# Performance work log

Measured on AMD Instinct MI355X. Metric: run time of the kernel, lower is better.

The kernel has to match this reference:

```python
import jax, jax.numpy as jnp
import numpy as np

C = 64
K = 3  # kernel_size
B, H, W = 8, 128, 128


def conv2d(x, w, b, pad, groups=1):
    y = jax.lax.conv_general_dilated(
        x, w, window_strides=(1, 1), padding=[(pad, pad), (pad, pad)],
        feature_group_count=groups, dimension_numbers=('NCHW', 'OIHW', 'NCHW'))
    return y + b[None, :, None, None]


def setup_inputs() -> dict:
    key = jax.random.key(0)
    ks = jax.random.split(key, 11)
    s3 = 1.0 / np.sqrt(C * 9)  # kaiming-ish scale for 3x3 convs
    inp = {
        'x':  jax.random.normal(ks[0], (B, C, H, W), jnp.float32),
        'w0': jax.random.normal(ks[1], (C, C, 3, 3), jnp.float32) * s3,
        'b0': jax.random.normal(ks[2], (C,), jnp.float32) * 0.01,
        'w1': jax.random.normal(ks[3], (C, 1, 3, 3), jnp.float32) * (1.0 / 3.0),  # depthwise
        'b1': jax.random.normal(ks[4], (C,), jnp.float32) * 0.01,
        'w2': jax.random.normal(ks[5], (1, 1, K), jnp.float32) * (1.0 / np.sqrt(K)),  # conv1d over channel axis
        'b2': jax.random.normal(ks[6], (1,), jnp.float32) * 0.01,
        'w3': jax.random.normal(ks[7], (C * K * K, C, 1, 1), jnp.float32) * (1.0 / np.sqrt(C)),  # 1x1 -> dynamic filters
        'b3': jax.random.normal(ks[8], (C * K * K,), jnp.float32) * 0.01,
        'wf': jax.random.normal(ks[9], (C, C, 3, 3), jnp.float32) * s3,
        'bf': jax.random.normal(ks[10], (C,), jnp.float32) * 0.01,
    }
    return inp


def reference(x, w0, b0, w1, b1, w2, b2, w3, b3, wf, bf):
    b, c, h, w = x.shape
    pre = x
    # conv0: dense 3x3
    x0 = conv2d(x, w0, b0, pad=1)
    # conv1: depthwise 3x3
    x1 = conv2d(x0, w1, b1, pad=1, groups=c)
    # ECA-style channel attention: global avg pool -> conv1d over channel dim
    m = jnp.mean(x0, axis=(2, 3))  # [b, c]
    x2 = jax.lax.conv_general_dilated(
        m[:, None, :], w2, window_strides=(1,), padding=[(K // 2, K // 2)],
        dimension_numbers=('NCH', 'OIH', 'NCH')) + b2[None, :, None]  # [b, 1, c]
    out = x1 + x2[:, 0, :, None, None]  # broadcast [b,c,1,1] over h,w
    # conv3: 1x1 producing per-pixel dynamic filters [b, c*9, h, w]
    fil = jnp.einsum('oc,bchw->bohw', w3[:, :, 0, 0], out) + b3[None, :, None, None]
    filter_x = fil.reshape(b, c, K * K, h, w)
    # unfold(x0): 3x3 patches, channel-major then row-major kernel positions
    xp = jnp.pad(x0, ((0, 0), (0, 0), (1, 1), (1, 1)))
    unfold_x = jnp.stack(
        [xp[:, :, i:i + h, j:j + w] for i in range(3) for j in range(3)], axis=2)  # [b,c,9,h,w]
    out = jnp.sum(unfold_x * filter_x, axis=2)  # per-pixel dynamic conv
    out = jnp.where(out >= 0, out, 0.2 * out)  # LeakyReLU(0.2)
    out = conv2d(out, wf, bf, pad=1) + pre
    return out
```

## Files before the change

kernel.cpp:

```cpp
#include <hip/hip_runtime.h>

#define BB 8
#define C 64
#define HH 128
#define WW 128
#define HW (HH*WW)

#define TS 72
#define NPX 324

typedef __attribute__((ext_vector_type(8))) short short8;
typedef __attribute__((ext_vector_type(4))) short short4v;
typedef __attribute__((ext_vector_type(4))) float f32x4;

__device__ inline unsigned short f2bf(float f) {
    union { float f; unsigned u; } v; v.f = f;
    unsigned r = v.u + 0x7fff + ((v.u >> 16) & 1);
    return (unsigned short)(r >> 16);
}
__device__ inline float bf2f(unsigned short h) {
    union { unsigned u; float f; } v; v.u = ((unsigned)h) << 16;
    return v.f;
}

__global__ __launch_bounds__(256) void prep_kernel(
    const float* __restrict__ w0, const float* __restrict__ wf,
    const float* __restrict__ w3, const float* __restrict__ b3,
    unsigned short* __restrict__ wb0, unsigned short* __restrict__ wbf,
    unsigned short* __restrict__ wb3, float* __restrict__ b3r,
    float* __restrict__ m)
{
    const int t = blockIdx.x * 256 + threadIdx.x;
    for (int i = t; i < C*C*9; i += 32*256) {
        int p = i % 9; int rest = i / 9; int ci = rest % C; int oc = rest / C;
        wb0[(p*C + oc)*C + ci] = f2bf(w0[i]);
        wbf[(p*C + oc)*C + ci] = f2bf(wf[i]);
    }
    for (int i = t; i < 9*C*C; i += 32*256) {
        int j = i >> 12, oc = (i >> 6) & 63, k = i & 63;
        wb3[i] = f2bf(w3[(oc*9 + j)*C + k]);
    }
    for (int i = t; i < 9*C; i += 32*256) {
        int j = i >> 6, oc = i & 63;
        b3r[i] = b3[oc*9 + j];
    }
    for (int i = t; i < BB*C; i += 32*256) m[i] = 0.f;
}

__global__ __launch_bounds__(512) void conv0_kernel(
    const float* __restrict__ x,
    const unsigned short* __restrict__ wb,
    const float* __restrict__ bias,
    unsigned short* __restrict__ x0g)
{
    __shared__ unsigned short tile[NPX*TS];
    const int b  = blockIdx.z;
    const int h0 = blockIdx.y * 16;
    const int w0 = blockIdx.x * 16;
    const int t  = threadIdx.x;

    {
        const int pxi = t & 63, g = t >> 6;
        for (int px = pxi; px < NPX; px += 64) {
            int th = px / 18, tw = px - th*18;
            int gh = h0 + th - 1, gw = w0 + tw - 1;
            short8 v = {0,0,0,0,0,0,0,0};
            if ((unsigned)gh < HH && (unsigned)gw < WW) {
                const float* sp = x + ((size_t)(b*C + g*8)*HW + gh*WW + gw);
#pragma unroll
                for (int k = 0; k < 8; ++k) v[k] = (short)f2bf(sp[k*HW]);
            }
            *(short8*)&tile[px*TS + g*8] = v;
        }
    }
    __syncthreads();

    const int wid = t >> 6, ln = t & 63;
    const int l15 = ln & 15, q = ln >> 4;

    f32x4 acc[2][4];
#pragma unroll
    for (int nt = 0; nt < 2; ++nt)
#pragma unroll
        for (int mt = 0; mt < 4; ++mt) acc[nt][mt] = (f32x4){0.f,0.f,0.f,0.f};

#pragma unroll
    for (int p = 0; p < 9; ++p) {
        const int dh = p / 3, dw = p % 3;
#pragma unroll
        for (int ks = 0; ks < 2; ++ks) {
            short8 af[4];
#pragma unroll
            for (int mt = 0; mt < 4; ++mt)
                af[mt] = *(const short8*)&wb[((size_t)(p*C) + mt*16 + l15)*C + ks*32 + q*8];
            short8 bf[2];
#pragma unroll
            for (int nt = 0; nt < 2; ++nt)
                bf[nt] = *(const short8*)&tile[((wid*2+nt+dh)*18 + l15 + dw)*TS + ks*32 + q*8];
#pragma unroll
            for (int nt = 0; nt < 2; ++nt)
#pragma unroll
                for (int mt = 0; mt < 4; ++mt)
                    acc[nt][mt] = __builtin_amdgcn_mfma_f32_16x16x32_bf16(
                        af[mt], bf[nt], acc[nt][mt], 0, 0, 0);
        }
    }

#pragma unroll
    for (int nt = 0; nt < 2; ++nt) {
        const int hh = h0 + wid*2 + nt;
        const size_t base = ((size_t)(b*HW) + hh*WW + w0 + l15)*C;
#pragma unroll
        for (int mt = 0; mt < 4; ++mt) {
            const int oc0 = mt*16 + q*4;
            const float4 bv = *(const float4*)&bias[oc0];
            unsigned u0 = (unsigned)f2bf(acc[nt][mt][0] + bv.x)
                        | ((unsigned)f2bf(acc[nt][mt][1] + bv.y) << 16);
            unsigned u1 = (unsigned)f2bf(acc[nt][mt][2] + bv.z)
                        | ((unsigned)f2bf(acc[nt][mt][3] + bv.w) << 16);
            uint2 uu; uu.x = u0; uu.y = u1;
            *(uint2*)&x0g[base + oc0] = uu;
        }
    }
}

__global__ __launch_bounds__(256) void mean_kernel(
    const unsigned short* __restrict__ x0, float* __restrict__ m)
{
    const int b = blockIdx.x >> 4, slice = blockIdx.x & 15;
    const int t = threadIdx.x;
    const int pxi = t >> 3, g = t & 7;
    const unsigned short* base = x0 + ((size_t)b*HW + slice*1024)*C + g*8;
    float s[8];
#pragma unroll
    for (int k = 0; k < 8; ++k) s[k] = 0.f;
    for (int it = 0; it < 32; ++it) {
        short8 v = *(const short8*)&base[(size_t)(it*32 + pxi)*C];
#pragma unroll
        for (int k = 0; k < 8; ++k) s[k] += bf2f((unsigned short)v[k]);
    }
    __shared__ float red[32][64];
#pragma unroll
    for (int k = 0; k < 8; ++k) red[pxi][g*8+k] = s[k];
    __syncthreads();
    if (t < 64) {
        float acc = 0.f;
        for (int i = 0; i < 32; ++i) acc += red[i][t];
        atomicAdd(&m[b*C + t], acc * (1.f/(float)HW));
    }
}

__global__ __launch_bounds__(512) void fused_dyn_kernel(
    const unsigned short* __restrict__ x0,
    const float* __restrict__ w1, const float* __restrict__ b1,
    const float* __restrict__ w2, const float* __restrict__ b2,
    const unsigned short* __restrict__ wb3,
    const float* __restrict__ b3r,
    const float* __restrict__ m,
    unsigned short* __restrict__ yg)
{
    __shared__ unsigned short tile[NPX*TS];
    __shared__ unsigned short alds[256*64];
    const int b  = blockIdx.z;
    const int h0 = blockIdx.y * 16;
    const int w0 = blockIdx.x * 16;
    const int t  = threadIdx.x;

    {
        const int pxi = t & 63, g = t >> 6;
        for (int px = pxi; px < NPX; px += 64) {
            int th = px / 18, tw = px - th*18;
            int gh = h0 + th - 1, gw = w0 + tw - 1;
            short8 v = {0,0,0,0,0,0,0,0};
            if ((unsigned)gh < HH && (unsigned)gw < WW)
                v = *(const short8*)&x0[((size_t)(b*HW) + gh*WW + gw)*C + g*8];
            *(short8*)&tile[px*TS + g*8] = v;
        }
    }
    __syncthreads();

    {
        const int px = t & 255, ghalf = t >> 8;
        const int r = px >> 4, cc = px & 15;
        const unsigned short* tb = tile + (r*18 + cc)*TS;
        const float w2a = w2[0], w2b = w2[1], w2c = w2[2], b2v = b2[0];
        const int sw = px & 7;
#pragma unroll
        for (int g = 0; g < 4; ++g) {
            const int octet = ghalf*4 + g;
            float dw8[8];
#pragma unroll
            for (int k = 0; k < 8; ++k) dw8[k] = 0.f;
#pragma unroll
            for (int j = 0; j < 9; ++j) {
                short8 v = *(const short8*)&tb[((j/3)*18 + (j%3))*TS + octet*8];
#pragma unroll
                for (int k = 0; k < 8; ++k)
                    dw8[k] = fmaf(w1[(octet*8+k)*9 + j],
                                  bf2f((unsigned short)v[k]), dw8[k]);
            }
            short8 o;
#pragma unroll
            for (int k = 0; k < 8; ++k) {
                const int c = octet*8 + k;
                const float mc = m[b*C + c];
                const float mp = (c > 0)  ? m[b*C + c - 1] : 0.f;
                const float mn = (c < 63) ? m[b*C + c + 1] : 0.f;
                const float att = fmaf(w2a, mp, fmaf(w2b, mc, fmaf(w2c, mn, b2v)));
                o[k] = (short)f2bf(dw8[k] + b1[c] + att);
            }
            *(short8*)&alds[px*64 + ((octet ^ sw) * 8)] = o;
        }
    }
    __syncthreads();

    const int wid = t >> 6, ln = t & 63;
    const int l15 = ln & 15, q = ln >> 4;
    const int rl0 = (wid & 3) * 4;
    const int ogh = wid >> 2;

    short8 pfrag[4][2];
#pragma unroll
    for (int nt = 0; nt < 4; ++nt) {
        const int p = (rl0 + nt)*16 + l15;
        const int psw = p & 7;
#pragma unroll
        for (int ks = 0; ks < 2; ++ks)
            pfrag[nt][ks] = *(const short8*)&alds[p*64 + (((ks*4 + q) ^ psw) * 8)];
    }

#pragma unroll
    for (int ogi = 0; ogi < 2; ++ogi) {
        const int og = ogh*2 + ogi;
        f32x4 yac[4];
#pragma unroll
        for (int nt = 0; nt < 4; ++nt) yac[nt] = (f32x4){0.f,0.f,0.f,0.f};

        for (int j = 0; j < 9; ++j) {
            const int dh = j / 3, dw = j - dh*3;
            const f32x4 seed = *(const f32x4*)&b3r[j*64 + og*16 + q*4];
            const size_t abase = ((size_t)(j*64 + og*16 + l15))*C;
            const short8 a0 = *(const short8*)&wb3[abase + q*8];
            const short8 a1 = *(const short8*)&wb3[abase + 32 + q*8];
#pragma unroll
            for (int nt = 0; nt < 4; ++nt) {
                f32x4 fil = __builtin_amdgcn_mfma_f32_16x16x32_bf16(
                    a0, pfrag[nt][0], seed, 0, 0, 0);
                fil = __builtin_amdgcn_mfma_f32_16x16x32_bf16(
                    a1, pfrag[nt][1], fil, 0, 0, 0);
                const short4v pv = *(const short4v*)
                    &tile[((rl0+nt+dh)*18 + l15 + dw)*TS + og*16 + q*4];
#pragma unroll
                for (int reg = 0; reg < 4; ++reg)
                    yac[nt][reg] = fmaf(fil[reg],
                        bf2f((unsigned short)pv[reg]), yac[nt][reg]);
            }
        }

#pragma unroll
        for (int nt = 0; nt < 4; ++nt) {
            const size_t base = ((size_t)(b*HW) + (h0+rl0+nt)*WW + w0 + l15)*C;
            f32x4 v = yac[nt];
#pragma unroll
            for (int reg = 0; reg < 4; ++reg)
                v[reg] = (v[reg] >= 0.f) ? v[reg] : 0.2f * v[reg];
            unsigned u0 = (unsigned)f2bf(v[0]) | ((unsigned)f2bf(v[1]) << 16);
            unsigned u1 = (unsigned)f2bf(v[2]) | ((unsigned)f2bf(v[3]) << 16);
            uint2 uu; uu.x = u0; uu.y = u1;
            *(uint2*)&yg[base + og*16 + q*4] = uu;
        }
    }
}

__global__ __launch_bounds__(512) void convf_kernel(
    const unsigned short* __restrict__ yg,
    const unsigned short* __restrict__ wb,
    const float* __restrict__ bias,
    const float* __restrict__ res,
    float* __restrict__ outg)
{
    __shared__ unsigned short tile[NPX*TS];
    const int b  = blockIdx.z;
    const int h0 = blockIdx.y * 16;
    const int w0 = blockIdx.x * 16;
    const int t  = threadIdx.x;

    {
        const int pxi = t & 63, g = t >> 6;
        for (int px = pxi; px < NPX; px += 64) {
            int th = px / 18, tw = px - th*18;
            int gh = h0 + th - 1, gw = w0 + tw - 1;
            short8 v = {0,0,0,0,0,0,0,0};
            if ((unsigned)gh < HH && (unsigned)gw < WW)
                v = *(const short8*)&yg[((size_t)(b*HW) + gh*WW + gw)*C + g*8];
            *(short8*)&tile[px*TS + g*8] = v;
        }
    }
    __syncthreads();

    const int wid = t >> 6, ln = t & 63;
    const int l15 = ln & 15, q = ln >> 4;

    f32x4 acc[2][4];
#pragma unroll
    for (int mg = 0; mg < 2; ++mg)
#pragma unroll
        for (int nt = 0; nt < 4; ++nt) acc[mg][nt] = (f32x4){0.f,0.f,0.f,0.f};

#pragma unroll
    for (int p = 0; p < 9; ++p) {
        const int dh = p / 3, dw = p % 3;
#pragma unroll
        for (int ks = 0; ks < 2; ++ks) {
            short8 bfrag[4];
#pragma unroll
            for (int nt = 0; nt < 4; ++nt)
                bfrag[nt] = *(const short8*)&wb[((size_t)(p*C) + nt*16 + l15)*C + ks*32 + q*8];
            short8 afrag[2];
#pragma unroll
            for (int mg = 0; mg < 2; ++mg)
                afrag[mg] = *(const short8*)&tile[((wid*2+mg+dh)*18 + l15 + dw)*TS + ks*32 + q*8];
#pragma unroll
            for (int mg = 0; mg < 2; ++mg)
#pragma unroll
                for (int nt = 0; nt < 4; ++nt)
                    acc[mg][nt] = __builtin_amdgcn_mfma_f32_16x16x32_bf16(
                        afrag[mg], bfrag[nt], acc[mg][nt], 0, 0, 0);
        }
    }

#pragma unroll
    for (int mg = 0; mg < 2; ++mg) {
        const int hh = h0 + wid*2 + mg;
#pragma unroll
        for (int nt = 0; nt < 4; ++nt) {
            const int oc = nt*16 + l15;
            const float bv = bias[oc];
            const size_t base = (size_t)(b*C + oc)*HW + hh*WW + w0 + q*4;
            const float4 rv = *(const float4*)&res[base];
            float4 ov;
            ov.x = acc[mg][nt][0] + bv + rv.x;
            ov.y = acc[mg][nt][1] + bv + rv.y;
            ov.z = acc[mg][nt][2] + bv + rv.z;
            ov.w = acc[mg][nt][3] + bv + rv.w;
            *(float4*)&outg[base] = ov;
        }
    }
}

extern "C" void kernel_launch(void* const* d_in, const int* in_sizes, int n_in,
                              void* d_out, int out_size, void* d_ws, size_t ws_size,
                              hipStream_t stream) {
    const float* x  = (const float*)d_in[0];
    const float* w0 = (const float*)d_in[1];
    const float* b0 = (const float*)d_in[2];
    const float* w1 = (const float*)d_in[3];
    const float* b1 = (const float*)d_in[4];
    const float* w2 = (const float*)d_in[5];
    const float* b2 = (const float*)d_in[6];
    const float* w3 = (const float*)d_in[7];
    const float* b3 = (const float*)d_in[8];
    const float* wf = (const float*)d_in[9];
    const float* bf = (const float*)d_in[10];
    float* out = (float*)d_out;

    unsigned short* x0  = (unsigned short*)d_ws;
    unsigned short* y   = x0  + (size_t)BB*HW*C;
    float*          m   = (float*)(y + (size_t)BB*HW*C);
    unsigned short* wb0 = (unsigned short*)(m + BB*C);
    unsigned short* wbf = wb0 + 9*C*C;
    unsigned short* wb3 = wbf + 9*C*C;
    float*          b3r = (float*)(wb3 + 9*C*C);

    prep_kernel<<<32, 256, 0, stream>>>(w0, wf, w3, b3, wb0, wbf, wb3, b3r, m);
    conv0_kernel<<<dim3(8,8,8), 512, 0, stream>>>(x, wb0, b0, x0);
    mean_kernel<<<128, 256, 0, stream>>>(x0, m);
    fused_dyn_kernel<<<dim3(8,8,8), 512, 0, stream>>>(
        x0, w1, b1, w2, b2, wb3, b3r, m, y);
    convf_kernel<<<dim3(8,8,8), 512, 0, stream>>>(y, wbf, bf, x, out);
}
```

Measured before the change: 246.5 us.

## Fuse channel mean into conv0, pre-convert input to NHWC bf16, retile convf

Adds a separate kernel that converts the NCHW fp32 input into NHWC bf16, so conv0 loads its halo tile with one vectorised read per pixel instead of eight strided fp32 reads. The channel-mean reduction moves into the conv0 epilogue using wave shuffles and an LDS reduction, which removes the standalone mean kernel and its re-read of x0. The sum is scaled by 1/HW later in the dynamic kernel. The final conv switches to 8x32 tiles so residual loads and output stores are contiguous across 32 columns, at the cost of a slightly larger halo tile and an extra pass over the input.

Result: no change. 248.2 us (+0.7%).

```diff
diff --git a/kernel.cpp b/kernel.cpp
--- a/kernel.cpp
+++ b/kernel.cpp
@@ -8,6 +8,7 @@
 
 #define TS 72
 #define NPX 324
+#define FNPX 340
 
 typedef __attribute__((ext_vector_type(8))) short short8;
 typedef __attribute__((ext_vector_type(4))) short short4v;
@@ -47,13 +48,31 @@
     for (int i = t; i < BB*C; i += 32*256) m[i] = 0.f;
 }
 
+__global__ __launch_bounds__(256) void nhwc_kernel(
+    const float* __restrict__ x, unsigned short* __restrict__ xb)
+{
+    const int px = blockIdx.x * 256 + threadIdx.x;
+    const int b = px >> 14, pin = px & 16383;
+    const float* sp = x + (size_t)b*C*HW + pin;
+    unsigned short* dp = xb + (size_t)px*C;
+#pragma unroll
+    for (int g = 0; g < 8; ++g) {
+        short8 o;
+#pragma unroll
+        for (int k = 0; k < 8; ++k) o[k] = (short)f2bf(sp[(size_t)(g*8+k)*HW]);
+        *(short8*)&dp[g*8] = o;
+    }
+}
+
 __global__ __launch_bounds__(512) void conv0_kernel(
-    const float* __restrict__ x,
+    const unsigned short* __restrict__ xb,
     const unsigned short* __restrict__ wb,
     const float* __restrict__ bias,
-    unsigned short* __restrict__ x0g)
+    unsigned short* __restrict__ x0g,
+    float* __restrict__ msum)
 {
     __shared__ unsigned short tile[NPX*TS];
+    __shared__ float red[8][64];
     const int b  = blockIdx.z;
     const int h0 = blockIdx.y * 16;
     const int w0 = blockIdx.x * 16;
@@ -65,11 +84,8 @@
             int th = px / 18, tw = px - th*18;
             int gh = h0 + th - 1, gw = w0 + tw - 1;
             short8 v = {0,0,0,0,0,0,0,0};
-            if ((unsigned)gh < HH && (unsigned)gw < WW) {
-                const float* sp = x + ((size_t)(b*C + g*8)*HW + gh*WW + gw);
-#pragma unroll
-                for (int k = 0; k < 8; ++k) v[k] = (short)f2bf(sp[k*HW]);
-            }
+            if ((unsigned)gh < HH && (unsigned)gw < WW)
+                v = *(const short8*)&xb[((size_t)(b*HW) + gh*WW + gw)*C + g*8];
             *(short8*)&tile[px*TS + g*8] = v;
         }
     }
@@ -122,31 +138,33 @@
             *(uint2*)&x0g[base + oc0] = uu;
         }
     }
-}
-
-__global__ __launch_bounds__(256) void mean_kernel(
-    const unsigned short* __restrict__ x0, float* __restrict__ m)
-{
-    const int b = blockIdx.x >> 4, slice = blockIdx.x & 15;
-    const int t = threadIdx.x;
-    const int pxi = t >> 3, g = t & 7;
-    const unsigned short* base = x0 + ((size_t)b*HW + slice*1024)*C + g*8;
-    float s[8];
-#pragma unroll
-    for (int k = 0; k < 8; ++k) s[k] = 0.f;
-    for (int it = 0; it < 32; ++it) {
-        short8 v = *(const short8*)&base[(size_t)(it*32 + pxi)*C];
-#pragma unroll
-        for (int k = 0; k < 8; ++k) s[k] += bf2f((unsigned short)v[k]);
-    }
-    __shared__ float red[32][64];
-#pragma unroll
-    for (int k = 0; k < 8; ++k) red[pxi][g*8+k] = s[k];
+
+    f32x4 s[4];
+#pragma unroll
+    for (int mt = 0; mt < 4; ++mt)
+#pragma unroll
+        for (int reg = 0; reg < 4; ++reg)
+            s[mt][reg] = acc[0][mt][reg] + acc[1][mt][reg];
+#pragma unroll
+    for (int mask = 1; mask < 16; mask <<= 1)
+#pragma unroll
+        for (int mt = 0; mt < 4; ++mt)
+#pragma unroll
+            for (int reg = 0; reg < 4; ++reg)
+                s[mt][reg] += __shfl_xor(s[mt][reg], mask);
+    if (l15 == 0) {
+#pragma unroll
+        for (int mt = 0; mt < 4; ++mt)
+#pragma unroll
+            for (int reg = 0; reg < 4; ++reg)
+                red[wid][mt*16 + q*4 + reg] = s[mt][reg];
+    }
     __syncthreads();
     if (t < 64) {
-        float acc = 0.f;
-        for (int i = 0; i < 32; ++i) acc += red[i][t];
-        atomicAdd(&m[b*C + t], acc * (1.f/(float)HW));
+        float tot = bias[t] * 256.f;
+#pragma unroll
+        for (int w = 0; w < 8; ++w) tot += red[w][t];
+        atomicAdd(&msum[b*C + t], tot);
     }
 }
 
@@ -184,6 +202,7 @@
         const int r = px >> 4, cc = px & 15;
         const unsigned short* tb = tile + (r*18 + cc)*TS;
         const float w2a = w2[0], w2b = w2[1], w2c = w2[2], b2v = b2[0];
+        const float inv = 1.f / (float)HW;
         const int sw = px & 7;
 #pragma unroll
         for (int g = 0; g < 4; ++g) {
@@ -203,9 +222,9 @@
 #pragma unroll
             for (int k = 0; k < 8; ++k) {
                 const int c = octet*8 + k;
-                const float mc = m[b*C + c];
-                const float mp = (c > 0)  ? m[b*C + c - 1] : 0.f;
-                const float mn = (c < 63) ? m[b*C + c + 1] : 0.f;
+                const float mc = m[b*C + c] * inv;
+                const float mp = (c > 0)  ? m[b*C + c - 1] * inv : 0.f;
+                const float mn = (c < 63) ? m[b*C + c + 1] * inv : 0.f;
                 const float att = fmaf(w2a, mp, fmaf(w2b, mc, fmaf(w2c, mn, b2v)));
                 o[k] = (short)f2bf(dw8[k] + b1[c] + att);
             }
@@ -279,16 +298,16 @@
     const float* __restrict__ res,
     float* __restrict__ outg)
 {
-    __shared__ unsigned short tile[NPX*TS];
+    __shared__ unsigned short tile[FNPX*TS];
     const int b  = blockIdx.z;
-    const int h0 = blockIdx.y * 16;
-    const int w0 = blockIdx.x * 16;
+    const int h0 = blockIdx.y * 8;
+    const int w0 = blockIdx.x * 32;
     const int t  = threadIdx.x;
 
     {
         const int pxi = t & 63, g = t >> 6;
-        for (int px = pxi; px < NPX; px += 64) {
-            int th = px / 18, tw = px - th*18;
+        for (int px = pxi; px < FNPX; px += 64) {
+            int th = px / 34, tw = px - th*34;
             int gh = h0 + th - 1, gw = w0 + tw - 1;
             short8 v = {0,0,0,0,0,0,0,0};
             if ((unsigned)gh < HH && (unsigned)gw < WW)
@@ -319,7 +338,7 @@
             short8 afrag[2];
 #pragma unroll
             for (int mg = 0; mg < 2; ++mg)
-                afrag[mg] = *(const short8*)&tile[((wid*2+mg+dh)*18 + l15 + dw)*TS + ks*32 + q*8];
+                afrag[mg] = *(const short8*)&tile[((wid+dh)*34 + mg*16 + l15 + dw)*TS + ks*32 + q*8];
 #pragma unroll
             for (int mg = 0; mg < 2; ++mg)
 #pragma unroll
@@ -331,12 +350,11 @@
 
 #pragma unroll
     for (int mg = 0; mg < 2; ++mg) {
-        const int hh = h0 + wid*2 + mg;
 #pragma unroll
         for (int nt = 0; nt < 4; ++nt) {
             const int oc = nt*16 + l15;
             const float bv = bias[oc];
-            const size_t base = (size_t)(b*C + oc)*HW + hh*WW + w0 + q*4;
+            const size_t base = (size_t)(b*C + oc)*HW + (h0+wid)*WW + w0 + mg*16 + q*4;
             const float4 rv = *(const float4*)&res[base];
             float4 ov;
             ov.x = acc[mg][nt][0] + bv + rv.x;
@@ -366,16 +384,17 @@
 
     unsigned short* x0  = (unsigned short*)d_ws;
     unsigned short* y   = x0  + (size_t)BB*HW*C;
-    float*          m   = (float*)(y + (size_t)BB*HW*C);
+    unsigned short* xb  = y   + (size_t)BB*HW*C;
+    float*          m   = (float*)(xb + (size_t)BB*HW*C);
     unsigned short* wb0 = (unsigned short*)(m + BB*C);
     unsigned short* wbf = wb0 + 9*C*C;
     unsigned short* wb3 = wbf + 9*C*C;
     float*          b3r = (float*)(wb3 + 9*C*C);
 
     prep_kernel<<<32, 256, 0, stream>>>(w0, wf, w3, b3, wb0, wbf, wb3, b3r, m);
-    conv0_kernel<<<dim3(8,8,8), 512, 0, stream>>>(x, wb0, b0, x0);
-    mean_kernel<<<128, 256, 0, stream>>>(x0, m);
+    nhwc_kernel<<<512, 256, 0, stream>>>(x, xb);
+    conv0_kernel<<<dim3(8,8,8), 512, 0, stream>>>(xb, wb0, b0, x0, m);
     fused_dyn_kernel<<<dim3(8,8,8), 512, 0, stream>>>(
         x0, w1, b1, w2, b2, wb3, b3r, m, y);
-    convf_kernel<<<dim3(8,8,8), 512, 0, stream>>>(y, wbf, bf, x, out);
-}
+    convf_kernel<<<dim3(4,16,8), 512, 0, stream>>>(y, wbf, bf, x, out);
+}
```
